# Kernel optimization log

Measured on AMD Instinct MI355X. Metric: run time of the kernel, lower is better.

## Reference

```python
import jax, jax.numpy as jnp
import numpy as np

LQ, LK, B, E, H = 1024, 1024, 8, 1024, 16


def setup_inputs() -> dict:
    key0 = jax.random.key(0)
    ks = jax.random.split(key0, 6)
    std = float(np.sqrt(2.0 / (E + E)))
    query = jax.random.normal(ks[0], (LQ, B, E), dtype=jnp.float32)
    key = jax.random.normal(ks[1], (LK, B, E), dtype=jnp.float32)
    attn_mask = jax.random.randint(ks[2], (B, LK), 0, 2).astype(bool)
    in_proj_weight_q = std * jax.random.normal(ks[3], (E, E), dtype=jnp.float32)
    in_proj_weight_kv = std * jax.random.normal(ks[4], (2 * E, E), dtype=jnp.float32)
    out_proj_weight = std * jax.random.normal(ks[5], (E, E), dtype=jnp.float32)
    return {
        "query": query,
        "key": key,
        "attn_mask": attn_mask,
        "in_proj_weight_q": in_proj_weight_q,
        "in_proj_weight_kv": in_proj_weight_kv,
        "out_proj_weight": out_proj_weight,
        "num_heads": H,
    }


def reference(query, key, attn_mask, in_proj_weight_q, in_proj_weight_kv, out_proj_weight, num_heads):
    Lq, Bs, Em = query.shape
    Lk = key.shape[0]
    Hd = Em // num_heads  # head_dim
    scaling = Hd ** (-0.5)

    # input projections: F.linear(x, W) == x @ W.T  (no bias)
    q = jnp.einsum("lbe,fe->lbf", query, in_proj_weight_q) * scaling
    kv = jnp.einsum("lbe,fe->lbf", key, in_proj_weight_kv)
    k, v = jnp.split(kv, 2, axis=-1)

    # [len, b, e] -> [b, h, len, d]
    def to_heads(x, L):
        return x.reshape(L, Bs, num_heads, Hd).transpose(1, 2, 0, 3)

    qh = to_heads(q, Lq)
    kh = to_heads(k, Lk)
    vh = to_heads(v, Lk)

    scores = jnp.einsum("bhqd,bhkd->bhqk", qh, kh)  # [B,H,Lq,Lk]
    neg = jnp.asarray(-1e9, scores.dtype)
    scores = jnp.where(attn_mask[:, None, None, :], neg, scores)
    attn = jax.nn.softmax(scores, axis=-1)  # coverage (dropout=0, eval)

    ctx = jnp.einsum("bhqk,bhkd->bhqd", attn, vh)  # [B,H,Lq,d]
    ctx = ctx.transpose(2, 0, 1, 3).reshape(Lq, Bs, Em)
    out = jnp.einsum("lbe,fe->lbf", ctx, out_proj_weight)
    return out, attn
```

## Files before the change

kernel.cpp:

```cpp
#include <hip/hip_runtime.h>
#include <hip/hip_bf16.h>
#include <cstdint>
#include <cstddef>

constexpr int LQc = 1024, LKc = 1024, Bc = 8, Ec = 1024, Hc = 16, Dc = 64;

typedef __bf16 bf16;
typedef __bf16 bf16x4 __attribute__((ext_vector_type(4)));
typedef __bf16 bf16x8 __attribute__((ext_vector_type(8)));
typedef float  f32x4  __attribute__((ext_vector_type(4)));

#define MFMA16(a, b, c) __builtin_amdgcn_mfma_f32_16x16x32_bf16((a), (b), (c), 0, 0, 0)
#define EXP2F(x) __builtin_amdgcn_exp2f(x)

__device__ __forceinline__ void gload_lds16(const bf16* g, bf16* l) {
  __builtin_amdgcn_global_load_lds((const __attribute__((address_space(1))) void*)g,
                                   (__attribute__((address_space(3))) void*)l, 16, 0, 0);
}

__global__ __launch_bounds__(256) void k_convert(const float* __restrict__ q,
                                                 const float* __restrict__ k,
                                                 const float* __restrict__ wq,
                                                 const float* __restrict__ wkv,
                                                 const float* __restrict__ wout,
                                                 bf16* __restrict__ dst) {
  const size_t i = ((size_t)blockIdx.x * 256 + threadIdx.x) * 8;
  const float* src; size_t off; float sc = 1.0f;
  if (i < 8388608)        { src = q;    off = i; sc = 0.18033688f; }
  else if (i < 16777216)  { src = k;    off = i - 8388608; }
  else if (i < 17825792)  { src = wq;   off = i - 16777216; }
  else if (i < 19922944)  { src = wkv;  off = i - 17825792; }
  else                    { src = wout; off = i - 19922944; }
  const f32x4 a = *reinterpret_cast<const f32x4*>(src + off);
  const f32x4 b = *reinterpret_cast<const f32x4*>(src + off + 4);
  bf16x8 o;
  o[0] = (bf16)(a.x * sc); o[1] = (bf16)(a.y * sc);
  o[2] = (bf16)(a.z * sc); o[3] = (bf16)(a.w * sc);
  o[4] = (bf16)(b.x * sc); o[5] = (bf16)(b.y * sc);
  o[6] = (bf16)(b.z * sc); o[7] = (bf16)(b.w * sc);
  *reinterpret_cast<bf16x8*>(dst + i) = o;
}

template <int MODE>
__global__ __launch_bounds__(256) void k_gemm(const bf16* __restrict__ Aq,
                                              const bf16* __restrict__ Ak,
                                              const bf16* __restrict__ Wq,
                                              const bf16* __restrict__ Wkv,
                                              bf16* __restrict__ qh,
                                              bf16* __restrict__ kh,
                                              bf16* __restrict__ vh,
                                              float* __restrict__ o_f) {
  __shared__ bf16 As[128 * 32];
  __shared__ bf16 Bs[128 * 32];

  const int tid  = threadIdx.x;
  const int lane = tid & 63, wave = tid >> 6;
  const int wm = wave & 1, wn = wave >> 1;

  const int cpx = gridDim.x >> 3;
  const int logical = (blockIdx.x & 7) * cpx + (blockIdx.x >> 3);
  const int bx = logical & 63, by = logical >> 6;
  const int m0 = bx * 128;

  const bf16* Ap;
  const bf16* Wp;
  bf16* Op = nullptr;
  if constexpr (MODE == 0) {
    if (by < 8)       { Ap = Aq; Wp = Wq  + (size_t)by * 131072;        Op = qh; }
    else if (by < 16) { Ap = Ak; Wp = Wkv + (size_t)(by - 8) * 131072;  Op = kh; }
    else              { Ap = Ak; Wp = Wkv + 1048576 + (size_t)(by - 16) * 131072; Op = vh; }
  } else {
    Ap = Aq; Wp = Wq + (size_t)by * 131072;
  }
  const int col0 = (by & 7) * 128;

  const int fr = lane & 15, fo = (lane >> 4) * 8;

  f32x4 acc[4][4] = {};

  const int srow = lane >> 2;
  const int scol = (lane & 3) * 8;
  const bf16* ga = Ap + (size_t)(m0 + wave * 32 + srow) * Ec + scol;
  const bf16* gb = Wp + (size_t)(wave * 32 + srow) * Ec + scol;
  bf16* lA = As + wave * 1024;
  bf16* lB = Bs + wave * 1024;

  for (int k0 = 0; k0 < Ec; k0 += 32) {
    gload_lds16(ga + k0, lA);
    gload_lds16(ga + k0 + 16 * Ec, lA + 512);
    gload_lds16(gb + k0, lB);
    gload_lds16(gb + k0 + 16 * Ec, lB + 512);
    __syncthreads();

    bf16x8 a[4], b[4];
#pragma unroll
    for (int i = 0; i < 4; ++i) {
      a[i] = *reinterpret_cast<const bf16x8*>(As + (wm * 64 + i * 16 + fr) * 32 + fo);
      b[i] = *reinterpret_cast<const bf16x8*>(Bs + (wn * 64 + i * 16 + fr) * 32 + fo);
    }
#pragma unroll
    for (int i = 0; i < 4; ++i)
#pragma unroll
      for (int j = 0; j < 4; ++j) acc[i][j] = MFMA16(a[i], b[j], acc[i][j]);
    __syncthreads();
  }

  const int rb = (lane >> 4) * 4;
#pragma unroll
  for (int i = 0; i < 4; ++i) {
#pragma unroll
    for (int j = 0; j < 4; ++j) {
      const int col = col0 + wn * 64 + j * 16 + fr;
#pragma unroll
      for (int r = 0; r < 4; ++r) {
        const int tok = m0 + wm * 64 + i * 16 + rb + r;
        const float val = acc[i][j][r];
        if constexpr (MODE == 0) {
          const int lq = tok >> 3, bb = tok & 7;
          const int h = col >> 6, dd = col & 63;
          Op[(((size_t)(bb * Hc + h)) * LQc + lq) * Dc + dd] = (bf16)val;
        } else {
          __builtin_nontemporal_store(val, o_f + (size_t)tok * Ec + col);
        }
      }
    }
  }
}

__global__ __launch_bounds__(256) void k_vtrans(const bf16* __restrict__ Vh,
                                                bf16* __restrict__ VhT) {
  __shared__ bf16 tile[64][72];
  const int bh = blockIdx.y;
  const int l0 = blockIdx.x * 64;
  const int r = threadIdx.x >> 3, c = (threadIdx.x & 7) * 8;
#pragma unroll
  for (int rr = 0; rr < 2; ++rr) {
    const int row = rr * 32 + r;
    *reinterpret_cast<bf16x8*>(&tile[row][c]) =
        *reinterpret_cast<const bf16x8*>(Vh + ((size_t)bh * LKc + l0 + row) * Dc + c);
  }
  __syncthreads();
#pragma unroll
  for (int rr = 0; rr < 2; ++rr) {
    const int d = rr * 32 + r;
    bf16x8 o;
#pragma unroll
    for (int j = 0; j < 8; ++j) o[j] = tile[c + j][d];
    *reinterpret_cast<bf16x8*>(VhT + ((size_t)bh * Dc + d) * LKc + l0 + c) = o;
  }
}

__global__ __launch_bounds__(256) void k_attn(const bf16* __restrict__ Qh,
                                              const bf16* __restrict__ Kh,
                                              const bf16* __restrict__ VhT,
                                              const int* __restrict__ mask,
                                              float* __restrict__ attn_out,
                                              bf16* __restrict__ ctx_out) {
  __shared__ bf16 sP[32][1032];
  __shared__ float smask[1024];
  __shared__ float psum[4][32];

  const int tid = threadIdx.x;
  const int lane = tid & 63, wave = tid >> 6;
  const int parity = (blockIdx.x >> 9) & 1;

  int flat = blockIdx.x;
  flat = (flat & 7) * 512 + (flat >> 3);
  const int bh = flat >> 5;
  const int q0 = (flat & 31) * 32;
  const int b = bh >> 4, h = bh & 15;
  const int fr = lane & 15, fo = (lane >> 4) * 8, rb = (lane >> 4) * 4;

#pragma unroll
  for (int c = tid; c < 1024; c += 256)
    smask[c] = mask[b * LKc + c] ? -1e9f : 0.0f;

  bf16x8 qf[2][2];
  const bf16* Qb = Qh + ((size_t)bh * LQc + q0) * Dc;
#pragma unroll
  for (int m = 0; m < 2; ++m)
#pragma unroll
    for (int kc = 0; kc < 2; ++kc)
      qf[m][kc] = *reinterpret_cast<const bf16x8*>(Qb + (size_t)(m * 16 + fr) * Dc + kc * 32 + fo);
  __syncthreads();

  const bf16* Kb = Kh + (size_t)bh * LKc * Dc;
  float s0 = 0.f, s1 = 0.f;
#pragma unroll 4
  for (int t = 0; t < 16; ++t) {
    const int n = (wave * 16 + t) * 16;
    const bf16* kp = Kb + (size_t)(n + fr) * Dc + fo;
    const bf16x8 kf0 = *reinterpret_cast<const bf16x8*>(kp);
    const bf16x8 kf1 = *reinterpret_cast<const bf16x8*>(kp + 32);
    f32x4 c0 = {}, c1 = {};
    c0 = MFMA16(kf0, qf[0][0], c0);
    c0 = MFMA16(kf1, qf[0][1], c0);
    c1 = MFMA16(kf0, qf[1][0], c1);
    c1 = MFMA16(kf1, qf[1][1], c1);
    const int kb = n + rb;
    const f32x4 madd = *reinterpret_cast<const f32x4*>(&smask[kb]);
    bf16x4 p0, p1;
#pragma unroll
    for (int r = 0; r < 4; ++r) {
      const float e0 = EXP2F(c0[r] + madd[r]);
      const float e1 = EXP2F(c1[r] + madd[r]);
      s0 += e0; s1 += e1;
      p0[r] = (bf16)e0; p1[r] = (bf16)e1;
    }
    *reinterpret_cast<bf16x4*>(&sP[fr][kb])      = p0;
    *reinterpret_cast<bf16x4*>(&sP[16 + fr][kb]) = p1;
  }
  s0 += __shfl_xor(s0, 16, 64); s0 += __shfl_xor(s0, 32, 64);
  s1 += __shfl_xor(s1, 16, 64); s1 += __shfl_xor(s1, 32, 64);
  if (lane < 16) {
    psum[wave][fr]      = s0;
    psum[wave][16 + fr] = s1;
  }
  __syncthreads();

  float* ap = attn_out + ((size_t)bh * LQc + q0) * LKc;
  const bf16* Vb = VhT + ((size_t)bh * Dc + wave * 16 + fr) * LKc;
  f32x4 cacc0 = {}, cacc1 = {};

  const int wrbase = wave * 8;
  const bool write_first = (((wave >> 1) & 1) ^ parity) == 0;

  if (write_first) {
#pragma unroll 2
    for (int rr = 0; rr < 8; ++rr) {
      const int r = wrbase + rr;
      const float rs = 1.0f / (psum[0][r] + psum[1][r] + psum[2][r] + psum[3][r]);
#pragma unroll
      for (int ch = 0; ch < 4; ++ch) {
        const bf16x4 v = *reinterpret_cast<const bf16x4*>(&sP[r][ch * 256 + lane * 4]);
        f32x4 p;
        p.x = (float)v.x * rs; p.y = (float)v.y * rs;
        p.z = (float)v.z * rs; p.w = (float)v.w * rs;
        __builtin_nontemporal_store(p,
            reinterpret_cast<f32x4*>(ap + (size_t)r * LKc + ch * 256 + lane * 4));
      }
    }
#pragma unroll 4
    for (int kc = 0; kc < 1024; kc += 32) {
      const bf16x8 vf  = *reinterpret_cast<const bf16x8*>(Vb + kc + fo);
      const bf16x8 pa0 = *reinterpret_cast<const bf16x8*>(&sP[fr][kc + fo]);
      const bf16x8 pa1 = *reinterpret_cast<const bf16x8*>(&sP[16 + fr][kc + fo]);
      cacc0 = MFMA16(pa0, vf, cacc0);
      cacc1 = MFMA16(pa1, vf, cacc1);
    }
  } else {
#pragma unroll 4
    for (int kc = 0; kc < 1024; kc += 32) {
      const bf16x8 vf  = *reinterpret_cast<const bf16x8*>(Vb + kc + fo);
      const bf16x8 pa0 = *reinterpret_cast<const bf16x8*>(&sP[fr][kc + fo]);
      const bf16x8 pa1 = *reinterpret_cast<const bf16x8*>(&sP[16 + fr][kc + fo]);
      cacc0 = MFMA16(pa0, vf, cacc0);
      cacc1 = MFMA16(pa1, vf, cacc1);
    }
#pragma unroll 2
    for (int rr = 0; rr < 8; ++rr) {
      const int r = wrbase + rr;
      const float rs = 1.0f / (psum[0][r] + psum[1][r] + psum[2][r] + psum[3][r]);
#pragma unroll
      for (int ch = 0; ch < 4; ++ch) {
        const bf16x4 v = *reinterpret_cast<const bf16x4*>(&sP[r][ch * 256 + lane * 4]);
        f32x4 p;
        p.x = (float)v.x * rs; p.y = (float)v.y * rs;
        p.z = (float)v.z * rs; p.w = (float)v.w * rs;
        __builtin_nontemporal_store(p,
            reinterpret_cast<f32x4*>(ap + (size_t)r * LKc + ch * 256 + lane * 4));
      }
    }
  }

  const int e = h * Dc + wave * 16 + fr;
#pragma unroll
  for (int r = 0; r < 4; ++r) {
    const int row0 = rb + r, row1 = 16 + rb + r;
    const float rs0 = 1.0f / (psum[0][row0] + psum[1][row0] + psum[2][row0] + psum[3][row0]);
    const float rs1 = 1.0f / (psum[0][row1] + psum[1][row1] + psum[2][row1] + psum[3][row1]);
    ctx_out[((size_t)(q0 + row0) * Bc + b) * Ec + e] = (bf16)(cacc0[r] * rs0);
    ctx_out[((size_t)(q0 + row1) * Bc + b) * Ec + e] = (bf16)(cacc1[r] * rs1);
  }
}

extern "C" void kernel_launch(void* const* d_in, const int* in_sizes, int n_in,
                              void* d_out, int out_size, void* d_ws, size_t ws_size,
                              hipStream_t stream) {
  const float* query = (const float*)d_in[0];
  const float* keyx  = (const float*)d_in[1];
  const int*   mask  = (const int*)d_in[2];
  const float* wq    = (const float*)d_in[3];
  const float* wkv   = (const float*)d_in[4];
  const float* wout  = (const float*)d_in[5];

  float* out  = (float*)d_out;
  float* attn = out + (size_t)LQc * Bc * Ec;

  bf16* cvt   = (bf16*)d_ws;
  bf16* q2    = cvt;
  bf16* k2    = q2   + 8388608;
  bf16* wqb   = k2   + 8388608;
  bf16* wkvb  = wqb  + 1048576;
  bf16* woutb = wkvb + 2097152;
  bf16* qh    = woutb + 1048576;
  bf16* kh    = qh   + 8388608;
  bf16* vh    = kh   + 8388608;
  bf16* vt    = q2;
  bf16* ctx   = k2;

  k_convert<<<10240, 256, 0, stream>>>(query, keyx, wq, wkv, wout, cvt);
  k_gemm<0><<<1536, 256, 0, stream>>>(q2, k2, wqb, wkvb, qh, kh, vh, nullptr);
  k_vtrans<<<dim3(16, 128), 256, 0, stream>>>(vh, vt);
  k_attn<<<4096, 256, 0, stream>>>(qh, kh, vt, mask, attn, ctx);
  k_gemm<2><<<512, 256, 0, stream>>>(ctx, nullptr, woutb, nullptr, nullptr, nullptr, nullptr, out);
}
```

Before: 295.7 us.

## Replace QKV projection GEMM with 256x256-tile double-buffered swizzled-LDS kernel

Adds a new QKV projection kernel with 512 threads, 256x256 output tiles, K-step 64, double-buffered LDS staging through direct global-to-LDS loads, and an XOR-swizzled LDS layout. Explicit vmcnt waits let the next tile's loads overlap the current tile's MFMAs. The larger tile raises arithmetic intensity and cuts global reloads of the operands. In exchange it uses 128KB of LDS per block (one block per CU despite the launch-bounds hint), launches 384 blocks, and needs many accumulator registers, which could limit occupancy or cause spills.

```diff
diff --git a/kernel.cpp b/kernel.cpp
--- a/kernel.cpp
+++ b/kernel.cpp
@@ -41,14 +41,115 @@
   *reinterpret_cast<bf16x8*>(dst + i) = o;
 }
 
+__global__ __launch_bounds__(512, 2) void k_gemm8(const bf16* __restrict__ Aq,
+                                                  const bf16* __restrict__ Ak,
+                                                  const bf16* __restrict__ Wq,
+                                                  const bf16* __restrict__ Wkv,
+                                                  bf16* __restrict__ qh,
+                                                  bf16* __restrict__ kh,
+                                                  bf16* __restrict__ vh) {
+  __shared__ bf16 lds[65536];
+
+  const int tid = threadIdx.x, lane = tid & 63, wave = tid >> 6;
+  const int wm = wave >> 2, wn = wave & 3;
+  const int fr = lane & 15, q4 = lane >> 4;
+
+  const int logical = (blockIdx.x & 7) * 48 + (blockIdx.x >> 3);
+  const int bx = logical & 31, by = logical >> 5;
+  const int m0 = bx * 256;
+
+  const bf16* Ap = (by < 4) ? Aq : Ak;
+  const bf16* Wp;
+  bf16* Op;
+  if (by < 4)      { Wp = Wq  + (size_t)by * 262144;              Op = qh; }
+  else if (by < 8) { Wp = Wkv + (size_t)(by - 4) * 262144;        Op = kh; }
+  else             { Wp = Wkv + 1048576 + (size_t)(by - 8) * 262144; Op = vh; }
+
+  const int srow = lane >> 3;
+  const int scol = ((lane & 7) ^ (srow & 7)) * 8;
+  const bf16* gA0 = Ap + (size_t)(m0 + wave * 16 + srow) * 1024 + scol;
+  const bf16* gW0 = Wp + (size_t)(wave * 16 + srow) * 1024 + scol;
+
+#define STAGE_A(nd, kt, h) do {                                        \
+    const bf16* s_ = gA0 + (size_t)(h) * 131072 + (kt) * 64;           \
+    bf16* d_ = lds + (nd) * 16384 + (h) * 8192 + wave * 1024;          \
+    gload_lds16(s_, d_); gload_lds16(s_ + 8192, d_ + 512);             \
+  } while (0)
+#define STAGE_B(nd, kt, h) do {                                        \
+    const bf16* s_ = gW0 + (size_t)(h) * 131072 + (kt) * 64;           \
+    bf16* d_ = lds + 32768 + (nd) * 16384 + (h) * 8192 + wave * 1024;  \
+    gload_lds16(s_, d_); gload_lds16(s_ + 8192, d_ + 512);             \
+  } while (0)
+
+  const int cs0 = ((q4) ^ (fr & 7)) * 8;
+  const int cs1 = cs0 ^ 32;
+
+  f32x4 acc[8][4] = {};
+  bf16x8 bfr[4][2];
+
+  STAGE_A(0, 0, 0); STAGE_A(0, 0, 1); STAGE_B(0, 0, 0); STAGE_B(0, 0, 1);
+
+#define COMPUTE_GROUP(d)                                                      \
+  {                                                                           \
+    const bf16* lb = lds + 32768 + (d) * 16384 + (wn >> 1) * 8192 +           \
+                     (wn & 1) * 4096;                                         \
+    _Pragma("unroll") for (int n = 0; n < 4; ++n) {                           \
+      bfr[n][0] = *(const bf16x8*)(lb + (n * 16 + fr) * 64 + cs0);            \
+      bfr[n][1] = *(const bf16x8*)(lb + (n * 16 + fr) * 64 + cs1);            \
+    }                                                                         \
+    const bf16* la = lds + (d) * 16384 + wm * 8192 + fr * 64;                 \
+    _Pragma("unroll") for (int qq = 0; qq < 4; ++qq) {                        \
+      bf16x8 af[2][2];                                                        \
+      _Pragma("unroll") for (int mm = 0; mm < 2; ++mm) {                      \
+        const int m_ = qq * 2 + mm;                                           \
+        af[mm][0] = *(const bf16x8*)(la + m_ * 1024 + cs0);                   \
+        af[mm][1] = *(const bf16x8*)(la + m_ * 1024 + cs1);                   \
+      }                                                                       \
+      _Pragma("unroll") for (int mm = 0; mm < 2; ++mm)                        \
+        _Pragma("unroll") for (int n = 0; n < 4; ++n) {                       \
+          acc[qq * 2 + mm][n] = MFMA16(af[mm][0], bfr[n][0], acc[qq * 2 + mm][n]); \
+          acc[qq * 2 + mm][n] = MFMA16(af[mm][1], bfr[n][1], acc[qq * 2 + mm][n]); \
+        }                                                                     \
+    }                                                                         \
+  }
+
+#pragma unroll 1
+  for (int g = 0; g < 15; ++g) {
+    const int d = g & 1, nd = d ^ 1;
+    STAGE_A(nd, g + 1, 0); STAGE_A(nd, g + 1, 1);
+    STAGE_B(nd, g + 1, 0); STAGE_B(nd, g + 1, 1);
+    asm volatile("s_waitcnt vmcnt(8)" ::: "memory");
+    asm volatile("s_barrier" ::: "memory");
+    COMPUTE_GROUP(d);
+    asm volatile("s_barrier" ::: "memory");
+  }
+  asm volatile("s_waitcnt vmcnt(0)" ::: "memory");
+  asm volatile("s_barrier" ::: "memory");
+  COMPUTE_GROUP(1);
+
+  const int rb = q4 * 4;
+#pragma unroll
+  for (int m = 0; m < 8; ++m) {
+#pragma unroll
+    for (int n = 0; n < 4; ++n) {
+      const int f = (by & 3) * 256 + wn * 64 + n * 16 + fr;
+      const int h = f >> 6, dd = f & 63;
+#pragma unroll
+      for (int r = 0; r < 4; ++r) {
+        const int tok = m0 + wm * 128 + m * 16 + rb + r;
+        const int lq = tok >> 3, bb = tok & 7;
+        Op[(((size_t)(bb * Hc + h)) * LQc + lq) * Dc + dd] = (bf16)acc[m][n][r];
+      }
+    }
+  }
+#undef STAGE_A
+#undef STAGE_B
+#undef COMPUTE_GROUP
+}
+
 template <int MODE>
 __global__ __launch_bounds__(256) void k_gemm(const bf16* __restrict__ Aq,
-                                              const bf16* __restrict__ Ak,
                                               const bf16* __restrict__ Wq,
-                                              const bf16* __restrict__ Wkv,
-                                              bf16* __restrict__ qh,
-                                              bf16* __restrict__ kh,
-                                              bf16* __restrict__ vh,
                                               float* __restrict__ o_f) {
   __shared__ bf16 As[128 * 32];
   __shared__ bf16 Bs[128 * 32];
@@ -62,16 +163,8 @@
   const int bx = logical & 63, by = logical >> 6;
   const int m0 = bx * 128;
 
-  const bf16* Ap;
-  const bf16* Wp;
-  bf16* Op = nullptr;
-  if constexpr (MODE == 0) {
-    if (by < 8)       { Ap = Aq; Wp = Wq  + (size_t)by * 131072;        Op = qh; }
-    else if (by < 16) { Ap = Ak; Wp = Wkv + (size_t)(by - 8) * 131072;  Op = kh; }
-    else              { Ap = Ak; Wp = Wkv + 1048576 + (size_t)(by - 16) * 131072; Op = vh; }
-  } else {
-    Ap = Aq; Wp = Wq + (size_t)by * 131072;
-  }
+  const bf16* Ap = Aq;
+  const bf16* Wp = Wq + (size_t)by * 131072;
   const int col0 = (by & 7) * 128;
 
   const int fr = lane & 15, fo = (lane >> 4) * 8;
@@ -114,14 +207,7 @@
 #pragma unroll
       for (int r = 0; r < 4; ++r) {
         const int tok = m0 + wm * 64 + i * 16 + rb + r;
-        const float val = acc[i][j][r];
-        if constexpr (MODE == 0) {
-          const int lq = tok >> 3, bb = tok & 7;
-          const int h = col >> 6, dd = col & 63;
-          Op[(((size_t)(bb * Hc + h)) * LQc + lq) * Dc + dd] = (bf16)val;
-        } else {
-          __builtin_nontemporal_store(val, o_f + (size_t)tok * Ec + col);
-        }
+        __builtin_nontemporal_store(acc[i][j][r], o_f + (size_t)tok * Ec + col);
       }
     }
   }
@@ -310,8 +396,8 @@
   bf16* ctx   = k2;
 
   k_convert<<<10240, 256, 0, stream>>>(query, keyx, wq, wkv, wout, cvt);
-  k_gemm<0><<<1536, 256, 0, stream>>>(q2, k2, wqb, wkvb, qh, kh, vh, nullptr);
+  k_gemm8<<<384, 512, 0, stream>>>(q2, k2, wqb, wkvb, qh, kh, vh);
   k_vtrans<<<dim3(16, 128), 256, 0, stream>>>(vh, vt);
   k_attn<<<4096, 256, 0, stream>>>(qh, kh, vt, mask, attn, ctx);
-  k_gemm<2><<<512, 256, 0, stream>>>(ctx, nullptr, woutb, nullptr, nullptr, nullptr, nullptr, out);
-}
+  k_gemm<2><<<512, 256, 0, stream>>>(ctx, woutb, out);
+}
```

New measurement: 292.3 us (median of 2 runs). Within noise of the previous version (-1.2%).

## Rewrite GEMM with 256x128 tiles, double-buffered LDS and XOR swizzle

Applied to the files above, without the earlier changes.

Replaces the 128x128 single-buffered GEMM with a 512-thread kernel computing 256x128 tiles over a K-step of 64. Global-to-LDS loads are double buffered, with the next stage issued before computing the current one and explicit vmcnt waits and barriers. An XOR swizzle on LDS columns is meant to avoid bank conflicts. The aim is to hide memory latency and halve the barriers per K element, at the cost of 96KB of LDS per block and hand-written waitcnt logic that depends on the exact number of loads in flight.

```diff
diff --git a/kernel.cpp b/kernel.cpp
--- a/kernel.cpp
+++ b/kernel.cpp
@@ -42,89 +42,116 @@
 }
 
 template <int MODE>
-__global__ __launch_bounds__(256) void k_gemm(const bf16* __restrict__ Aq,
-                                              const bf16* __restrict__ Ak,
-                                              const bf16* __restrict__ Wq,
-                                              const bf16* __restrict__ Wkv,
-                                              bf16* __restrict__ qh,
-                                              bf16* __restrict__ kh,
-                                              bf16* __restrict__ vh,
-                                              float* __restrict__ o_f) {
-  __shared__ bf16 As[128 * 32];
-  __shared__ bf16 Bs[128 * 32];
-
-  const int tid  = threadIdx.x;
-  const int lane = tid & 63, wave = tid >> 6;
-  const int wm = wave & 1, wn = wave >> 1;
+__global__ __launch_bounds__(512, 2) void k_gemm8(const bf16* __restrict__ Aq,
+                                                  const bf16* __restrict__ Ak,
+                                                  const bf16* __restrict__ Wq,
+                                                  const bf16* __restrict__ Wkv,
+                                                  bf16* __restrict__ qh,
+                                                  bf16* __restrict__ kh,
+                                                  bf16* __restrict__ vh,
+                                                  float* __restrict__ o_f) {
+  __shared__ bf16 lds[49152];
+
+  const int tid = threadIdx.x, lane = tid & 63, wave = tid >> 6;
+  const int wm = wave >> 1, wn = wave & 1;
+  const int fr = lane & 15, q4 = lane >> 4;
 
   const int cpx = gridDim.x >> 3;
   const int logical = (blockIdx.x & 7) * cpx + (blockIdx.x >> 3);
-  const int bx = logical & 63, by = logical >> 6;
-  const int m0 = bx * 128;
+  const int bx = logical & 31, by = logical >> 5;
+  const int m0 = bx * 256;
 
   const bf16* Ap;
   const bf16* Wp;
   bf16* Op = nullptr;
   if constexpr (MODE == 0) {
-    if (by < 8)       { Ap = Aq; Wp = Wq  + (size_t)by * 131072;        Op = qh; }
-    else if (by < 16) { Ap = Ak; Wp = Wkv + (size_t)(by - 8) * 131072;  Op = kh; }
-    else              { Ap = Ak; Wp = Wkv + 1048576 + (size_t)(by - 16) * 131072; Op = vh; }
+    Ap = (by < 8) ? Aq : Ak;
+    if (by < 8)       { Wp = Wq  + (size_t)by * 131072;               Op = qh; }
+    else if (by < 16) { Wp = Wkv + (size_t)(by - 8) * 131072;         Op = kh; }
+    else              { Wp = Wkv + 1048576 + (size_t)(by - 16) * 131072; Op = vh; }
   } else {
     Ap = Aq; Wp = Wq + (size_t)by * 131072;
   }
-  const int col0 = (by & 7) * 128;
-
-  const int fr = lane & 15, fo = (lane >> 4) * 8;
+
+  const int srow = lane >> 3;
+  const int scol = ((lane & 7) ^ srow) * 8;
+  const bf16* gA0 = Ap + (size_t)(m0 + wave * 32 + srow) * 1024 + scol;
+  const bf16* gW0 = Wp + (size_t)(wave * 16 + srow) * 1024 + scol;
+
+#define STAGE(nd, kt) do {                                                  \
+    const bf16* sa_ = gA0 + (kt) * 64;                                      \
+    bf16* da_ = lds + (nd) * 16384 + wave * 2048;                           \
+    gload_lds16(sa_,                 da_);                                  \
+    gload_lds16(sa_ + 8 * 1024,      da_ + 512);                            \
+    gload_lds16(sa_ + 16 * 1024,     da_ + 1024);                           \
+    gload_lds16(sa_ + 24 * 1024,     da_ + 1536);                           \
+    const bf16* sb_ = gW0 + (kt) * 64;                                      \
+    bf16* db_ = lds + 32768 + (nd) * 8192 + wave * 1024;                    \
+    gload_lds16(sb_,                 db_);                                  \
+    gload_lds16(sb_ + 8 * 1024,      db_ + 512);                            \
+  } while (0)
+
+  const int cs0 = (q4 ^ (fr & 7)) * 8;
+  const int cs1 = cs0 ^ 32;
 
   f32x4 acc[4][4] = {};
 
-  const int srow = lane >> 2;
-  const int scol = (lane & 3) * 8;
-  const bf16* ga = Ap + (size_t)(m0 + wave * 32 + srow) * Ec + scol;
-  const bf16* gb = Wp + (size_t)(wave * 32 + srow) * Ec + scol;
-  bf16* lA = As + wave * 1024;
-  bf16* lB = Bs + wave * 1024;
-
-  for (int k0 = 0; k0 < Ec; k0 += 32) {
-    gload_lds16(ga + k0, lA);
-    gload_lds16(ga + k0 + 16 * Ec, lA + 512);
-    gload_lds16(gb + k0, lB);
-    gload_lds16(gb + k0 + 16 * Ec, lB + 512);
-    __syncthreads();
-
-    bf16x8 a[4], b[4];
-#pragma unroll
-    for (int i = 0; i < 4; ++i) {
-      a[i] = *reinterpret_cast<const bf16x8*>(As + (wm * 64 + i * 16 + fr) * 32 + fo);
-      b[i] = *reinterpret_cast<const bf16x8*>(Bs + (wn * 64 + i * 16 + fr) * 32 + fo);
-    }
-#pragma unroll
-    for (int i = 0; i < 4; ++i)
-#pragma unroll
-      for (int j = 0; j < 4; ++j) acc[i][j] = MFMA16(a[i], b[j], acc[i][j]);
-    __syncthreads();
-  }
-
-  const int rb = (lane >> 4) * 4;
+#define COMPUTE_GROUP(d)                                                      \
+  {                                                                           \
+    bf16x8 bfr[4][2];                                                         \
+    const bf16* lb = lds + 32768 + (d) * 8192 + (wn * 64 + fr) * 64;          \
+    _Pragma("unroll") for (int n = 0; n < 4; ++n) {                           \
+      bfr[n][0] = *(const bf16x8*)(lb + n * 1024 + cs0);                      \
+      bfr[n][1] = *(const bf16x8*)(lb + n * 1024 + cs1);                      \
+    }                                                                         \
+    const bf16* la = lds + (d) * 16384 + (wm * 64 + fr) * 64;                 \
+    _Pragma("unroll") for (int i = 0; i < 4; ++i) {                           \
+      bf16x8 af0 = *(const bf16x8*)(la + i * 1024 + cs0);                     \
+      bf16x8 af1 = *(const bf16x8*)(la + i * 1024 + cs1);                     \
+      _Pragma("unroll") for (int n = 0; n < 4; ++n) {                         \
+        acc[i][n] = MFMA16(af0, bfr[n][0], acc[i][n]);                        \
+        acc[i][n] = MFMA16(af1, bfr[n][1], acc[i][n]);                        \
+      }                                                                       \
+    }                                                                         \
+  }
+
+  STAGE(0, 0);
+#pragma unroll 1
+  for (int g = 0; g < 15; ++g) {
+    const int d = g & 1, nd = d ^ 1;
+    STAGE(nd, g + 1);
+    asm volatile("s_waitcnt vmcnt(6)" ::: "memory");
+    asm volatile("s_barrier" ::: "memory");
+    COMPUTE_GROUP(d);
+    asm volatile("s_barrier" ::: "memory");
+  }
+  asm volatile("s_waitcnt vmcnt(0)" ::: "memory");
+  asm volatile("s_barrier" ::: "memory");
+  COMPUTE_GROUP(1);
+
+  const int rb = q4 * 4;
 #pragma unroll
   for (int i = 0; i < 4; ++i) {
 #pragma unroll
-    for (int j = 0; j < 4; ++j) {
-      const int col = col0 + wn * 64 + j * 16 + fr;
+    for (int n = 0; n < 4; ++n) {
 #pragma unroll
       for (int r = 0; r < 4; ++r) {
         const int tok = m0 + wm * 64 + i * 16 + rb + r;
-        const float val = acc[i][j][r];
+        const float val = acc[i][n][r];
         if constexpr (MODE == 0) {
+          const int f = (by & 7) * 128 + wn * 64 + n * 16 + fr;
+          const int h = f >> 6, dd = f & 63;
           const int lq = tok >> 3, bb = tok & 7;
-          const int h = col >> 6, dd = col & 63;
           Op[(((size_t)(bb * Hc + h)) * LQc + lq) * Dc + dd] = (bf16)val;
         } else {
+          const int col = by * 128 + wn * 64 + n * 16 + fr;
           __builtin_nontemporal_store(val, o_f + (size_t)tok * Ec + col);
         }
       }
     }
   }
+#undef STAGE
+#undef COMPUTE_GROUP
 }
 
 __global__ __launch_bounds__(256) void k_vtrans(const bf16* __restrict__ Vh,
@@ -310,8 +337,8 @@
   bf16* ctx   = k2;
 
   k_convert<<<10240, 256, 0, stream>>>(query, keyx, wq, wkv, wout, cvt);
-  k_gemm<0><<<1536, 256, 0, stream>>>(q2, k2, wqb, wkvb, qh, kh, vh, nullptr);
+  k_gemm8<0><<<768, 512, 0, stream>>>(q2, k2, wqb, wkvb, qh, kh, vh, nullptr);
   k_vtrans<<<dim3(16, 128), 256, 0, stream>>>(vh, vt);
   k_attn<<<4096, 256, 0, stream>>>(qh, kh, vt, mask, attn, ctx);
-  k_gemm<2><<<512, 256, 0, stream>>>(ctx, nullptr, woutb, nullptr, nullptr, nullptr, nullptr, out);
-}
+  k_gemm8<2><<<256, 512, 0, stream>>>(ctx, nullptr, woutb, nullptr, nullptr, nullptr, nullptr, out);
+}
```

Result: no change. 293.6 us (-0.7%).
